# Kernel tuning notes

Hardware: AMD Instinct MI355X
Metric: run time of the kernel (lower is better)

## Reference

```python
import jax, jax.numpy as jnp
import numpy as np

DIM = 384
HEAD_DIM = 32
NUM_HEADS = DIM // HEAD_DIM
SCALE = HEAD_DIM ** -0.5


def setup_inputs() -> dict:
    key = jax.random.key(0)
    k1, k2, k3, k4 = jax.random.split(key, 4)
    x = jax.random.normal(k1, (8, DIM, 32, 32), dtype=jnp.float32)
    # torch nn.Linear stores weight as [out_features, in_features]
    W_qkv = jax.random.normal(k2, (3 * DIM, DIM), dtype=jnp.float32) * (DIM ** -0.5)
    W_proj = jax.random.normal(k3, (DIM, DIM), dtype=jnp.float32) * (DIM ** -0.5)
    b_proj = jax.random.normal(k4, (DIM,), dtype=jnp.float32) * 0.01
    return {"x": x, "W_qkv": W_qkv, "W_proj": W_proj, "b_proj": b_proj}


def reference(x, W_qkv, W_proj, b_proj):
    B, C, H, W = x.shape
    N = H * W
    # flatten spatial -> tokens: (B, N, C)
    xt = x.reshape(B, C, N).transpose(0, 2, 1)
    # qkv projection (no bias): (B, N, 3C)
    qkv = jnp.einsum('bnc,oc->bno', xt, W_qkv)
    qkv = qkv.reshape(B, N, 3, NUM_HEADS, HEAD_DIM).transpose(2, 0, 3, 1, 4)
    q, k, v = qkv[0], qkv[1], qkv[2]  # each (B, h, N, d)
    attn = jnp.einsum('bhnd,bhmd->bhnm', q * SCALE, k)  # (B, h, N, N)
    attn = jax.nn.softmax(attn, axis=-1)
    out = jnp.einsum('bhnm,bhmd->bhnd', attn, v)  # (B, h, N, d)
    out = out.transpose(0, 2, 1, 3).reshape(B, N, C)
    out = jnp.einsum('bnc,oc->bno', out, W_proj) + b_proj
    # back to (B, C, H, W)
    return out.transpose(0, 2, 1).reshape(B, C, H, W)
```

## Files before the change

### kernel.cpp

```cpp
#include <hip/hip_runtime.h>
#include <hip/hip_bf16.h>

#define DIM   384
#define HD    32
#define NH    12
#define NT    1024
#define BATCH 8
#define C2 0.2550347244197545f
#define M2 11.541560327111707f


typedef short shortx8 __attribute__((ext_vector_type(8)));
typedef float floatx4 __attribute__((ext_vector_type(4)));

#define GLD_LDS(gp, lp) \
    __builtin_amdgcn_global_load_lds((__attribute__((address_space(1))) const void*)(gp), \
                                     (__attribute__((address_space(3))) void*)(lp), 16, 0, 0)

static __device__ __forceinline__ unsigned short f2bf(float f) {
    unsigned int u = __float_as_uint(f);
    u += 0x7fffu + ((u >> 16) & 1u);
    return (unsigned short)(u >> 16);
}

template <int NA, int NB>
static __device__ __forceinline__ void ldfrag(shortx8 (&A)[NA], shortx8 (&B)[NB],
                                              const unsigned short* ab,
                                              const unsigned short* bb, int ks) {
#pragma unroll
    for (int s = 0; s < NA; s++) A[s] = *(const shortx8*)(ab + s * 6144 + ks * 512);
#pragma unroll
    for (int s = 0; s < NB; s++) B[s] = *(const shortx8*)(bb + s * 6144 + ks * 512);
}
template <int NA, int NB>
static __device__ __forceinline__ void mmblk(floatx4 (&acc)[NA][NB],
                                             const shortx8 (&A)[NA], const shortx8 (&B)[NB]) {
#pragma unroll
    for (int sm = 0; sm < NA; sm++)
#pragma unroll
        for (int sn = 0; sn < NB; sn++)
            acc[sm][sn] = __builtin_amdgcn_mfma_f32_16x16x32_bf16(A[sm], B[sn], acc[sm][sn], 0, 0, 0);
}

__global__ __launch_bounds__(256) void k_pre(const float* __restrict__ x,
                                             const float* __restrict__ wq,
                                             const float* __restrict__ wp,
                                             unsigned short* __restrict__ xtf,
                                             unsigned short* __restrict__ wqf,
                                             unsigned short* __restrict__ wpf) {
    const int bid = blockIdx.x;
    if (bid < 3072) {
        __shared__ float t[32][33];
        const int xb_ = bid & 31, kstep = (bid >> 5) % 12, b = bid / 384;
        const int n0 = xb_ * 32;
        const int tid = threadIdx.x;
        const int tx = tid & 31, ty = tid >> 5;
        const float* xb = x + ((size_t)b * DIM + kstep * 32) * NT + n0;
#pragma unroll
        for (int i = 0; i < 4; i++)
            t[ty + 8 * i][tx] = xb[(size_t)(ty + 8 * i) * NT + tx];
        __syncthreads();
        const int mtl = tid >> 7, kq = (tid >> 5) & 3, rem = tid & 31;
        const int mrow = rem >> 1, krH = rem & 1;
        ushort4 p;
        p.x = f2bf(t[kq * 8 + krH * 4 + 0][mtl * 16 + mrow]);
        p.y = f2bf(t[kq * 8 + krH * 4 + 1][mtl * 16 + mrow]);
        p.z = f2bf(t[kq * 8 + krH * 4 + 2][mtl * 16 + mrow]);
        p.w = f2bf(t[kq * 8 + krH * 4 + 3][mtl * 16 + mrow]);
        const size_t mtile = ((size_t)b * 1024 + n0) / 16 + mtl;
        const size_t off = ((mtile * 12 + kstep) * 4 + kq) * 128 + mrow * 8 + krH * 4;
        *(ushort4*)(xtf + off) = p;
    } else {
        const int tid = (bid - 3072) * 256 + threadIdx.x;
        const float* src; unsigned short* dst; int ci;
        if (tid < 110592) { ci = tid; src = wq; dst = wqf; }
        else              { ci = tid - 110592; src = wp; dst = wpf; }
        const int krH = ci & 1, orow = (ci >> 1) & 15, quad = (ci >> 5) & 3;
        const int t2 = ci >> 7, kstep = t2 % 12, ntile = t2 / 12;
        const int row = ntile * 16 + orow, col = kstep * 32 + quad * 8 + krH * 4;
        const float4 v = *(const float4*)(src + (size_t)row * DIM + col);
        ushort4 p;
        p.x = f2bf(v.x); p.y = f2bf(v.y); p.z = f2bf(v.z); p.w = f2bf(v.w);
        *(ushort4*)(dst + (size_t)ci * 4) = p;
    }
}

__global__ __launch_bounds__(256, 2) void k_qkv(const unsigned short* __restrict__ xtf,
                                                const unsigned short* __restrict__ wqf,
                                                unsigned short* __restrict__ qb,
                                                unsigned short* __restrict__ kb,
                                                unsigned short* __restrict__ vt) {
    const int lane = threadIdx.x & 63, w = threadIdx.x >> 6;
    const int quad = lane >> 4, l16 = lane & 15;
    const int m0 = blockIdx.x * 128 + (w & 1) * 64;
    const int n0 = blockIdx.y * 128 + (w >> 1) * 64;
    floatx4 acc[4][4] = {};
    const unsigned short* abase = xtf + ((size_t)(m0 >> 4) * 12 * 4 + quad) * 128 + l16 * 8;
    const unsigned short* bbase = wqf + ((size_t)(n0 >> 4) * 12 * 4 + quad) * 128 + l16 * 8;
    shortx8 A0[4], B0[4], A1[4], B1[4], A2[4], B2[4];
    ldfrag(A0, B0, abase, bbase, 0);
    ldfrag(A1, B1, abase, bbase, 1);
#pragma unroll
    for (int ks = 0; ks < 12; ks += 3) {
        if (ks + 2 < 12) ldfrag(A2, B2, abase, bbase, ks + 2);
        mmblk(acc, A0, B0);
        if (ks + 3 < 12) ldfrag(A0, B0, abase, bbase, ks + 3);
        mmblk(acc, A1, B1);
        if (ks + 4 < 12) ldfrag(A1, B1, abase, bbase, ks + 4);
        mmblk(acc, A2, B2);
    }
    const int bi = m0 >> 10;
#pragma unroll
    for (int sn = 0; sn < 4; sn++) {
        const int o = n0 + sn * 16 + l16;
        const int which = (o >= 2 * DIM) ? 2 : (o >= DIM ? 1 : 0);
        const int rem = o - which * DIM;
        const int h = rem >> 5, d = rem & 31;
        const int hi = bi * NH + h;
#pragma unroll
        for (int sm = 0; sm < 4; sm++) {
#pragma unroll
            for (int r = 0; r < 4; r++) {
                const int n = (m0 + sm * 16 + quad * 4 + r) & 1023;
                const unsigned short val = f2bf(acc[sm][sn][r]);
                if (which == 0)      qb[((size_t)hi * NT + n) * HD + d] = val;
                else if (which == 1) kb[((size_t)hi * NT + n) * HD + d] = val;
                else                 vt[((size_t)hi * HD + d) * NT + n] = val;
            }
        }
    }
}

__global__ __launch_bounds__(256) void k_attn(const unsigned short* __restrict__ qb,
                                              const unsigned short* __restrict__ kb,
                                              const unsigned short* __restrict__ vt,
                                              unsigned short* __restrict__ aoutf) {
    __shared__ __align__(16) unsigned short frag[2][8][4][512];
    const int lane = threadIdx.x & 63, w = threadIdx.x >> 6;
    const int quad = lane >> 4, l16 = lane & 15;
    const int g = blockIdx.x & 7, j = blockIdx.x >> 3;
    const int hi = g * 12 + j % 12;
    const int q0 = ((j / 12) * 4 + w) * 32;
    const unsigned short* Q = qb + (size_t)hi * NT * HD;
    const unsigned short* K = kb + (size_t)hi * NT * HD;
    const unsigned short* V = vt + (size_t)hi * HD * NT;

    const shortx8 qfA = *(const shortx8*)(Q + (size_t)(q0 + l16) * HD + quad * 8);
    const shortx8 qfB = *(const shortx8*)(Q + (size_t)(q0 + 16 + l16) * HD + quad * 8);
    const int krow = (l16 >> 2) * 8 + (l16 & 3);
    const unsigned short* gsrc0;
    if (w == 0)      gsrc0 = K + (size_t)krow * HD + quad * 8;
    else if (w == 1) gsrc0 = K + (size_t)(krow + 4) * HD + quad * 8;
    else if (w == 2) gsrc0 = V + (size_t)l16 * NT + quad * 8;
    else             gsrc0 = V + (size_t)(16 + l16) * NT + quad * 8;
    const int gstep = (w < 2) ? 32 * HD : 32;

    const shortx8 ones = {16256, 16256, 16256, 16256, 16256, 16256, 16256, 16256};
    floatx4 oloA = {}, ohiA = {}, dsA = {};
    floatx4 oloB = {}, ohiB = {}, dsB = {};
    const floatx4 zero = {};

#pragma unroll
    for (int t = 0; t < 8; t++)
        GLD_LDS(gsrc0 + (size_t)t * gstep, &frag[0][t][w][0]);
    __syncthreads();

    for (int p = 0; p < 4; p++) {
        const int pb = p & 1;
        if (p < 3) {
#pragma unroll
            for (int t = 0; t < 8; t++)
                GLD_LDS(gsrc0 + (size_t)((p + 1) * 8 + t) * gstep, &frag[pb ^ 1][t][w][0]);
        }
#pragma unroll
        for (int t = 0; t < 8; t++) {
            const unsigned short* fb = &frag[pb][t][0][0];
            const shortx8 kf0 = *(const shortx8*)(fb + 0 * 512 + lane * 8);
            const shortx8 kf1 = *(const shortx8*)(fb + 1 * 512 + lane * 8);
            const shortx8 vlo = *(const shortx8*)(fb + 2 * 512 + lane * 8);
            const shortx8 vhi = *(const shortx8*)(fb + 3 * 512 + lane * 8);
            const floatx4 sA0 = __builtin_amdgcn_mfma_f32_16x16x32_bf16(kf0, qfA, zero, 0, 0, 0);
            const floatx4 sA1 = __builtin_amdgcn_mfma_f32_16x16x32_bf16(kf1, qfA, zero, 0, 0, 0);
            const floatx4 sB0 = __builtin_amdgcn_mfma_f32_16x16x32_bf16(kf0, qfB, zero, 0, 0, 0);
            const floatx4 sB1 = __builtin_amdgcn_mfma_f32_16x16x32_bf16(kf1, qfB, zero, 0, 0, 0);
            float eA[8], eB[8];
#pragma unroll
            for (int r = 0; r < 4; r++) {
                eA[r]     = __builtin_amdgcn_exp2f(fmaf(sA0[r], C2, -M2));
                eA[4 + r] = __builtin_amdgcn_exp2f(fmaf(sA1[r], C2, -M2));
                eB[r]     = __builtin_amdgcn_exp2f(fmaf(sB0[r], C2, -M2));
                eB[4 + r] = __builtin_amdgcn_exp2f(fmaf(sB1[r], C2, -M2));
            }
            union { shortx8 s8; __hip_bfloat162 h[4]; } pA, pB;
#pragma unroll
            for (int i = 0; i < 4; i++) {
                pA.h[i] = __float22bfloat162_rn(make_float2(eA[2 * i], eA[2 * i + 1]));
                pB.h[i] = __float22bfloat162_rn(make_float2(eB[2 * i], eB[2 * i + 1]));
            }
            oloA = __builtin_amdgcn_mfma_f32_16x16x32_bf16(pA.s8, vlo, oloA, 0, 0, 0);
            ohiA = __builtin_amdgcn_mfma_f32_16x16x32_bf16(pA.s8, vhi, ohiA, 0, 0, 0);
            dsA  = __builtin_amdgcn_mfma_f32_16x16x32_bf16(pA.s8, ones, dsA, 0, 0, 0);
            oloB = __builtin_amdgcn_mfma_f32_16x16x32_bf16(pB.s8, vlo, oloB, 0, 0, 0);
            ohiB = __builtin_amdgcn_mfma_f32_16x16x32_bf16(pB.s8, vhi, ohiB, 0, 0, 0);
            dsB  = __builtin_amdgcn_mfma_f32_16x16x32_bf16(pB.s8, ones, dsB, 0, 0, 0);
        }
        __syncthreads();
    }
    const int bi = hi / NH, h = hi % NH;
    const size_t mt0 = (size_t)bi * 64 + (q0 >> 4);
    const int kqlo = l16 >> 3, kr = l16 & 7;
    unsigned short* pAp = aoutf + (mt0 * 12 + h) * 512 + kr;
    unsigned short* pBp = aoutf + ((mt0 + 1) * 12 + h) * 512 + kr;
#pragma unroll
    for (int r = 0; r < 4; r++) {
        const int mrow8 = (quad * 4 + r) * 8;
        const float invA = 1.0f / dsA[r], invB = 1.0f / dsB[r];
        pAp[kqlo * 128 + mrow8]       = f2bf(oloA[r] * invA);
        pAp[(2 + kqlo) * 128 + mrow8] = f2bf(ohiA[r] * invA);
        pBp[kqlo * 128 + mrow8]       = f2bf(oloB[r] * invB);
        pBp[(2 + kqlo) * 128 + mrow8] = f2bf(ohiB[r] * invB);
    }
}

__global__ __launch_bounds__(256, 2) void k_proj(const unsigned short* __restrict__ aoutf,
                                                 const unsigned short* __restrict__ wpf,
                                                 const float* __restrict__ bias,
                                                 float* __restrict__ out) {
    const int lane = threadIdx.x & 63, w = threadIdx.x >> 6;
    const int quad = lane >> 4, l16 = lane & 15;
    const int m0 = blockIdx.x * 64;
    const int n0 = blockIdx.y * 128 + w * 32;
    floatx4 acc[4][2] = {};
    const unsigned short* abase = aoutf + ((size_t)(m0 >> 4) * 12 * 4 + quad) * 128 + l16 * 8;
    const unsigned short* bbase = wpf + ((size_t)(n0 >> 4) * 12 * 4 + quad) * 128 + l16 * 8;
    shortx8 A0[4], B0[2], A1[4], B1[2], A2[4], B2[2];
    ldfrag(A0, B0, abase, bbase, 0);
    ldfrag(A1, B1, abase, bbase, 1);
#pragma unroll
    for (int ks = 0; ks < 12; ks += 3) {
        if (ks + 2 < 12) ldfrag(A2, B2, abase, bbase, ks + 2);
        mmblk(acc, A0, B0);
        if (ks + 3 < 12) ldfrag(A0, B0, abase, bbase, ks + 3);
        mmblk(acc, A1, B1);
        if (ks + 4 < 12) ldfrag(A1, B1, abase, bbase, ks + 4);
        mmblk(acc, A2, B2);
    }
    const int bi = m0 >> 10;
#pragma unroll
    for (int sn = 0; sn < 2; sn++) {
        const int o = n0 + sn * 16 + l16;
        const float bv = bias[o];
        float* orow = out + ((size_t)bi * DIM + o) * NT;
#pragma unroll
        for (int sm = 0; sm < 4; sm++) {
            const int nb = (m0 + sm * 16 + quad * 4) & 1023;
            float4 pack;
            pack.x = acc[sm][sn][0] + bv;
            pack.y = acc[sm][sn][1] + bv;
            pack.z = acc[sm][sn][2] + bv;
            pack.w = acc[sm][sn][3] + bv;
            *(float4*)(orow + nb) = pack;
        }
    }
}

extern "C" void kernel_launch(void* const* d_in, const int* in_sizes, int n_in,
                              void* d_out, int out_size, void* d_ws, size_t ws_size,
                              hipStream_t stream) {
    const float* x     = (const float*)d_in[0];
    const float* wqkv  = (const float*)d_in[1];
    const float* wproj = (const float*)d_in[2];
    const float* bias  = (const float*)d_in[3];
    float* out = (float*)d_out;

    unsigned short* xtf  = (unsigned short*)d_ws;
    unsigned short* qb   = xtf + 3145728;
    unsigned short* kb   = qb + 3145728;
    unsigned short* vt   = kb + 3145728;
    unsigned short* wqf  = vt + 3145728;
    unsigned short* wpf  = wqf + 442368;
    unsigned short* aoutf = xtf;

    k_pre<<<3648, 256, 0, stream>>>(x, wqkv, wproj, xtf, wqf, wpf);
    k_qkv<<<dim3(64, 9), 256, 0, stream>>>(xtf, wqf, qb, kb, vt);
    k_attn<<<768, 256, 0, stream>>>(qb, kb, vt, aoutf);
    k_proj<<<dim3(128, 3), 256, 0, stream>>>(aoutf, wpf, bias, out);
}
```

Baseline: 131.0 us.

## Pre-swizzle K/V into MFMA fragment layout and retile QKV/proj GEMMs

The QKV kernel now writes K and V directly in the per-32-key fragment order the attention kernel consumes. Each attention wave can then stream one contiguous 1KB fragment per step with global_load_lds instead of gathering strided K rows and transposed V columns. The attention LDS buffer is halved, with 4 key tiles per stage across 8 stages, and launch bounds are raised to 3 blocks per CU. The QKV and projection GEMMs use smaller per-wave tiles, with more blocks and two-deep register prefetch, to improve occupancy at the cost of less data reuse and scattered stores in the QKV epilogue.

```diff
diff --git a/kernel.cpp b/kernel.cpp
--- a/kernel.cpp
+++ b/kernel.cpp
@@ -85,75 +85,75 @@
     }
 }
 
-__global__ __launch_bounds__(256, 2) void k_qkv(const unsigned short* __restrict__ xtf,
+__global__ __launch_bounds__(256, 3) void k_qkv(const unsigned short* __restrict__ xtf,
                                                 const unsigned short* __restrict__ wqf,
                                                 unsigned short* __restrict__ qb,
-                                                unsigned short* __restrict__ kb,
-                                                unsigned short* __restrict__ vt) {
+                                                unsigned short* __restrict__ kvf) {
     const int lane = threadIdx.x & 63, w = threadIdx.x >> 6;
     const int quad = lane >> 4, l16 = lane & 15;
     const int m0 = blockIdx.x * 128 + (w & 1) * 64;
-    const int n0 = blockIdx.y * 128 + (w >> 1) * 64;
-    floatx4 acc[4][4] = {};
-    const unsigned short* abase = xtf + ((size_t)(m0 >> 4) * 12 * 4 + quad) * 128 + l16 * 8;
-    const unsigned short* bbase = wqf + ((size_t)(n0 >> 4) * 12 * 4 + quad) * 128 + l16 * 8;
-    shortx8 A0[4], B0[4], A1[4], B1[4], A2[4], B2[4];
+    const int n0 = blockIdx.y * 96 + (w >> 1) * 48;
+    floatx4 acc[4][3] = {};
+    const unsigned short* abase = xtf + ((size_t)(m0 >> 4) * 48 + quad) * 128 + l16 * 8;
+    const unsigned short* bbase = wqf + ((size_t)(n0 >> 4) * 48 + quad) * 128 + l16 * 8;
+    shortx8 A0[4], B0[3], A1[4], B1[3];
     ldfrag(A0, B0, abase, bbase, 0);
-    ldfrag(A1, B1, abase, bbase, 1);
-#pragma unroll
-    for (int ks = 0; ks < 12; ks += 3) {
-        if (ks + 2 < 12) ldfrag(A2, B2, abase, bbase, ks + 2);
+#pragma unroll
+    for (int ks = 0; ks < 12; ks += 2) {
+        if (ks + 1 < 12) ldfrag(A1, B1, abase, bbase, ks + 1);
         mmblk(acc, A0, B0);
-        if (ks + 3 < 12) ldfrag(A0, B0, abase, bbase, ks + 3);
+        if (ks + 2 < 12) ldfrag(A0, B0, abase, bbase, ks + 2);
         mmblk(acc, A1, B1);
-        if (ks + 4 < 12) ldfrag(A1, B1, abase, bbase, ks + 4);
-        mmblk(acc, A2, B2);
     }
     const int bi = m0 >> 10;
 #pragma unroll
-    for (int sn = 0; sn < 4; sn++) {
+    for (int sn = 0; sn < 3; sn++) {
         const int o = n0 + sn * 16 + l16;
         const int which = (o >= 2 * DIM) ? 2 : (o >= DIM ? 1 : 0);
         const int rem = o - which * DIM;
         const int h = rem >> 5, d = rem & 31;
-        const int hi = bi * NH + h;
+        const size_t hi = (size_t)bi * NH + h;
 #pragma unroll
         for (int sm = 0; sm < 4; sm++) {
 #pragma unroll
             for (int r = 0; r < 4; r++) {
                 const int n = (m0 + sm * 16 + quad * 4 + r) & 1023;
                 const unsigned short val = f2bf(acc[sm][sn][r]);
-                if (which == 0)      qb[((size_t)hi * NT + n) * HD + d] = val;
-                else if (which == 1) kb[((size_t)hi * NT + n) * HD + d] = val;
-                else                 vt[((size_t)hi * HD + d) * NT + n] = val;
+                if (which == 0) {
+                    qb[(hi * NT + n) * HD + d] = val;
+                } else if (which == 1) {
+                    const int key = n & 31;
+                    const int kf_ = ((key & 7) < 4) ? 0 : 1;
+                    const int kk = key - 4 * kf_;
+                    const int l16p = ((kk >> 3) << 2) | (kk & 3);
+                    const int pos = (l16p + 16 * (d >> 3)) * 8 + (d & 7);
+                    kvf[((hi * 32 + (n >> 5)) * 4 + kf_) * 512 + pos] = val;
+                } else {
+                    const int f = 2 + (d >> 4);
+                    const int ln = (d & 15) + 16 * ((n & 31) >> 3);
+                    const int pos = ln * 8 + (n & 7);
+                    kvf[((hi * 32 + (n >> 5)) * 4 + f) * 512 + pos] = val;
+                }
             }
         }
     }
 }
 
-__global__ __launch_bounds__(256) void k_attn(const unsigned short* __restrict__ qb,
-                                              const unsigned short* __restrict__ kb,
-                                              const unsigned short* __restrict__ vt,
-                                              unsigned short* __restrict__ aoutf) {
-    __shared__ __align__(16) unsigned short frag[2][8][4][512];
+__global__ __launch_bounds__(256, 3) void k_attn(const unsigned short* __restrict__ qb,
+                                                 const unsigned short* __restrict__ kvf,
+                                                 unsigned short* __restrict__ aoutf) {
+    __shared__ __align__(16) unsigned short frag[2][4][4][512];
     const int lane = threadIdx.x & 63, w = threadIdx.x >> 6;
     const int quad = lane >> 4, l16 = lane & 15;
     const int g = blockIdx.x & 7, j = blockIdx.x >> 3;
     const int hi = g * 12 + j % 12;
     const int q0 = ((j / 12) * 4 + w) * 32;
     const unsigned short* Q = qb + (size_t)hi * NT * HD;
-    const unsigned short* K = kb + (size_t)hi * NT * HD;
-    const unsigned short* V = vt + (size_t)hi * HD * NT;
 
     const shortx8 qfA = *(const shortx8*)(Q + (size_t)(q0 + l16) * HD + quad * 8);
     const shortx8 qfB = *(const shortx8*)(Q + (size_t)(q0 + 16 + l16) * HD + quad * 8);
-    const int krow = (l16 >> 2) * 8 + (l16 & 3);
-    const unsigned short* gsrc0;
-    if (w == 0)      gsrc0 = K + (size_t)krow * HD + quad * 8;
-    else if (w == 1) gsrc0 = K + (size_t)(krow + 4) * HD + quad * 8;
-    else if (w == 2) gsrc0 = V + (size_t)l16 * NT + quad * 8;
-    else             gsrc0 = V + (size_t)(16 + l16) * NT + quad * 8;
-    const int gstep = (w < 2) ? 32 * HD : 32;
+    const unsigned short* gsrc = kvf + ((size_t)hi * 32 * 4 + w) * 512 + lane * 8;
+    const int gstep = 4 * 512;
 
     const shortx8 ones = {16256, 16256, 16256, 16256, 16256, 16256, 16256, 16256};
     floatx4 oloA = {}, ohiA = {}, dsA = {};
@@ -161,19 +161,19 @@
     const floatx4 zero = {};
 
 #pragma unroll
-    for (int t = 0; t < 8; t++)
-        GLD_LDS(gsrc0 + (size_t)t * gstep, &frag[0][t][w][0]);
+    for (int t = 0; t < 4; t++)
+        GLD_LDS(gsrc + (size_t)t * gstep, &frag[0][t][w][0]);
     __syncthreads();
 
-    for (int p = 0; p < 4; p++) {
+    for (int p = 0; p < 8; p++) {
         const int pb = p & 1;
-        if (p < 3) {
-#pragma unroll
-            for (int t = 0; t < 8; t++)
-                GLD_LDS(gsrc0 + (size_t)((p + 1) * 8 + t) * gstep, &frag[pb ^ 1][t][w][0]);
-        }
-#pragma unroll
-        for (int t = 0; t < 8; t++) {
+        if (p < 7) {
+#pragma unroll
+            for (int t = 0; t < 4; t++)
+                GLD_LDS(gsrc + (size_t)((p + 1) * 4 + t) * gstep, &frag[pb ^ 1][t][w][0]);
+        }
+#pragma unroll
+        for (int t = 0; t < 4; t++) {
             const unsigned short* fb = &frag[pb][t][0][0];
             const shortx8 kf0 = *(const shortx8*)(fb + 0 * 512 + lane * 8);
             const shortx8 kf1 = *(const shortx8*)(fb + 1 * 512 + lane * 8);
@@ -222,28 +222,25 @@
     }
 }
 
-__global__ __launch_bounds__(256, 2) void k_proj(const unsigned short* __restrict__ aoutf,
+__global__ __launch_bounds__(256, 3) void k_proj(const unsigned short* __restrict__ aoutf,
                                                  const unsigned short* __restrict__ wpf,
                                                  const float* __restrict__ bias,
                                                  float* __restrict__ out) {
     const int lane = threadIdx.x & 63, w = threadIdx.x >> 6;
     const int quad = lane >> 4, l16 = lane & 15;
-    const int m0 = blockIdx.x * 64;
-    const int n0 = blockIdx.y * 128 + w * 32;
-    floatx4 acc[4][2] = {};
-    const unsigned short* abase = aoutf + ((size_t)(m0 >> 4) * 12 * 4 + quad) * 128 + l16 * 8;
-    const unsigned short* bbase = wpf + ((size_t)(n0 >> 4) * 12 * 4 + quad) * 128 + l16 * 8;
-    shortx8 A0[4], B0[2], A1[4], B1[2], A2[4], B2[2];
+    const int m0 = blockIdx.x * 64 + (w & 1) * 32;
+    const int n0 = blockIdx.y * 64 + (w >> 1) * 32;
+    floatx4 acc[2][2] = {};
+    const unsigned short* abase = aoutf + ((size_t)(m0 >> 4) * 48 + quad) * 128 + l16 * 8;
+    const unsigned short* bbase = wpf + ((size_t)(n0 >> 4) * 48 + quad) * 128 + l16 * 8;
+    shortx8 A0[2], B0[2], A1[2], B1[2];
     ldfrag(A0, B0, abase, bbase, 0);
-    ldfrag(A1, B1, abase, bbase, 1);
-#pragma unroll
-    for (int ks = 0; ks < 12; ks += 3) {
-        if (ks + 2 < 12) ldfrag(A2, B2, abase, bbase, ks + 2);
+#pragma unroll
+    for (int ks = 0; ks < 12; ks += 2) {
+        if (ks + 1 < 12) ldfrag(A1, B1, abase, bbase, ks + 1);
         mmblk(acc, A0, B0);
-        if (ks + 3 < 12) ldfrag(A0, B0, abase, bbase, ks + 3);
+        if (ks + 2 < 12) ldfrag(A0, B0, abase, bbase, ks + 2);
         mmblk(acc, A1, B1);
-        if (ks + 4 < 12) ldfrag(A1, B1, abase, bbase, ks + 4);
-        mmblk(acc, A2, B2);
     }
     const int bi = m0 >> 10;
 #pragma unroll
@@ -252,7 +249,7 @@
         const float bv = bias[o];
         float* orow = out + ((size_t)bi * DIM + o) * NT;
 #pragma unroll
-        for (int sm = 0; sm < 4; sm++) {
+        for (int sm = 0; sm < 2; sm++) {
             const int nb = (m0 + sm * 16 + quad * 4) & 1023;
             float4 pack;
             pack.x = acc[sm][sn][0] + bv;
@@ -275,14 +272,13 @@
 
     unsigned short* xtf  = (unsigned short*)d_ws;
     unsigned short* qb   = xtf + 3145728;
-    unsigned short* kb   = qb + 3145728;
-    unsigned short* vt   = kb + 3145728;
-    unsigned short* wqf  = vt + 3145728;
+    unsigned short* kvf  = qb + 3145728;
+    unsigned short* wqf  = kvf + 6291456;
     unsigned short* wpf  = wqf + 442368;
     unsigned short* aoutf = xtf;
 
     k_pre<<<3648, 256, 0, stream>>>(x, wqkv, wproj, xtf, wqf, wpf);
-    k_qkv<<<dim3(64, 9), 256, 0, stream>>>(xtf, wqf, qb, kb, vt);
-    k_attn<<<768, 256, 0, stream>>>(qb, kb, vt, aoutf);
-    k_proj<<<dim3(128, 3), 256, 0, stream>>>(aoutf, wpf, bias, out);
-}
+    k_qkv<<<dim3(64, 12), 256, 0, stream>>>(xtf, wqf, qb, kvf);
+    k_attn<<<768, 256, 0, stream>>>(qb, kvf, aoutf);
+    k_proj<<<dim3(128, 6), 256, 0, stream>>>(aoutf, wpf, bias, out);
+}
```

New measurement: 122.6 us. -6.4%, faster.
